# Kernel optimization log

Hardware: AMD Instinct MI355X
Metric: run time of the kernel (lower is better)

## Reference

```python
import jax, jax.numpy as jnp
import numpy as np

# sizes
N, B, NPG = 8192, 8, 1024          # total nodes, graphs, nodes per graph (equal-size graphs)
D, H, DH, L = 256, 8, 32, 2        # hidden, heads, head dim, layers
IN_C, OUT_D, E, DFF = 128, 64, 262144, 512
EPS = 1e-5


def setup_inputs() -> dict:
    key = jax.random.key(0)
    ks = jax.random.split(key, 20)
    p = lambda i, shp: jax.random.normal(ks[i], shp, jnp.float32) * 0.05
    return dict(
        x=jax.random.normal(ks[0], (N, IN_C), jnp.float32),
        edge_index=jax.random.randint(ks[1], (2, E), 0, N),
        batch=jnp.arange(N, dtype=jnp.int32) // NPG,  # sorted, equal-size graphs
        w_in=p(2, (D, IN_C)), b_in=p(3, (D,)),
        sage_wl=p(4, (L, D, D)), sage_bl=p(5, (L, D)), sage_wr=p(6, (L, D, D)),
        attn_iw=p(7, (L, 3 * D, D)), attn_ib=p(8, (L, 3 * D)),
        attn_ow=p(9, (L, D, D)), attn_ob=p(10, (L, D)),
        n1_w=jnp.ones((L, D)), n1_b=jnp.zeros((L, D)),
        n2_w=jnp.ones((L, D)), n2_b=jnp.zeros((L, D)),
        n3_w=jnp.ones((L, D)), n3_b=jnp.zeros((L, D)),
        mlp_w1=p(11, (L, DFF, D)), mlp_b1=p(12, (L, DFF)),
        mlp_w2=p(13, (L, D, DFF)), mlp_b2=p(14, (L, D)),
        bn_w=jnp.ones((L, D)), bn_b=jnp.zeros((L, D)),
        w_out=p(15, (OUT_D, D)), b_out=p(16, (OUT_D,)),
    )


def _bn(h, w, b):
    # BatchNorm1d over nodes (training-mode batch statistics, biased var)
    m = h.mean(0)
    v = jnp.mean((h - m) ** 2, axis=0)
    return (h - m) * jax.lax.rsqrt(v + EPS) * w + b


def _forward(x, edge_index, batch, w_in, b_in, sage_wl, sage_bl, sage_wr,
             attn_iw, attn_ib, attn_ow, attn_ob, n1_w, n1_b, n2_w, n2_b,
             n3_w, n3_b, mlp_w1, mlp_b1, mlp_w2, mlp_b2, bn_w, bn_b, w_out, b_out):
    src, dst = edge_index[0], edge_index[1]
    deg = jax.ops.segment_sum(jnp.ones((E,), jnp.float32), dst, num_segments=N)
    inv_deg = (1.0 / jnp.clip(deg, 1.0))[:, None]
    scale = 1.0 / np.sqrt(DH)

    h = x @ w_in.T + b_in  # in_proj Linear  [N, D]
    for l in range(L):
        # --- GPSConv: local SAGEConv (mean aggr) + residual + norm1 ---
        agg = jax.ops.segment_sum(h[src], dst, num_segments=N) * inv_deg
        loc = agg @ sage_wl[l].T + sage_bl[l] + h @ sage_wr[l].T
        loc = _bn(loc + h, n1_w[l], n1_b[l])
        # --- GPSConv: dense per-graph multi-head self-attention + residual + norm2 ---
        hd = h.reshape(B, NPG, D)  # to_dense_batch (no padding: equal graph sizes)
        qkv = hd @ attn_iw[l].T + attn_ib[l]  # [B, n, 3D]
        q, k, v = jnp.split(qkv, 3, axis=-1)
        sh = lambda t: t.reshape(B, NPG, H, DH).transpose(0, 2, 1, 3)  # [B, H, n, DH]
        a = jax.nn.softmax(jnp.einsum('bhqd,bhkd->bhqk', sh(q) * scale, sh(k)), axis=-1)
        o = jnp.einsum('bhqk,bhkd->bhqd', a, sh(v)).transpose(0, 2, 1, 3).reshape(B, NPG, D)
        o = (o @ attn_ow[l].T + attn_ob[l]).reshape(N, D)
        glob = _bn(o + h, n2_w[l], n2_b[l])
        # --- GPSConv: sum branches, MLP residual, norm3 ---
        out = loc + glob
        out = out + jax.nn.relu(out @ mlp_w1[l].T + mlp_b1[l]) @ mlp_w2[l].T + mlp_b2[l]
        out = _bn(out, n3_w[l], n3_b[l])
        # --- outer GPS: BatchNorm + relu + (dropout=eval) + residual ---
        h = h + jax.nn.relu(_bn(out, bn_w[l], bn_b[l]))
    pooled = h.reshape(B, NPG, D).mean(axis=1)  # global_mean_pool over sorted equal-size graphs
    return pooled @ w_out.T + b_out  # [B, OUT_D]


def reference(x, edge_index, batch, w_in, b_in, sage_wl, sage_bl, sage_wr,
              attn_iw, attn_ib, attn_ow, attn_ob, n1_w, n1_b, n2_w, n2_b,
              n3_w, n3_b, mlp_w1, mlp_b1, mlp_w2, mlp_b2, bn_w, bn_b, w_out, b_out):
    return _forward(x, edge_index, batch, w_in, b_in, sage_wl, sage_bl, sage_wr,
                    attn_iw, attn_ib, attn_ow, attn_ob, n1_w, n1_b, n2_w, n2_b,
                    n3_w, n3_b, mlp_w1, mlp_b1, mlp_w2, mlp_b2, bn_w, bn_b, w_out, b_out)
```

## Files before the change

kernel.cpp:

```cpp
#include <hip/hip_runtime.h>
#include <hip/hip_bf16.h>

#define N_NODES 8192
#define BGRAPH 8
#define NPG 1024
#define DIM 256
#define NH 8
#define DHEAD 32
#define NLAYERS 2
#define INC 128
#define OUTD 64
#define NEDGE 262144
#define DFF 512
#define EPS 1e-5f

typedef __attribute__((ext_vector_type(4))) float f32x4;
typedef __attribute__((ext_vector_type(8))) short s16x8;
typedef __attribute__((ext_vector_type(4))) ushort u16x4;

__device__ __forceinline__ float b2f(ushort u){
  unsigned v = ((unsigned)u) << 16;
  return __builtin_bit_cast(float, v);
}
__device__ __forceinline__ ushort f2b(float f){
  unsigned u = __builtin_bit_cast(unsigned, f);
  u += 0x7fffu + ((u >> 16) & 1u);
  return (ushort)(u >> 16);
}
__device__ __forceinline__ ushort f2b_trunc(float f){
  return (ushort)(__builtin_bit_cast(unsigned, f) >> 16);
}
__device__ __forceinline__ void gload16(const void* g, void* l){
  __builtin_amdgcn_global_load_lds(
    (const __attribute__((address_space(1))) void*)g,
    (__attribute__((address_space(3))) void*)l,
    16, 0, 0);
}

#define CX  1048576
#define CWI (CX+32768)
#define CSW (CWI+262144)
#define CIW (CSW+393216)
#define COW (CIW+131072)
#define CW1 (COW+262144)
#define CW2 (CW1+262144)
#define NCAST (CW2/256)
__global__ void k_setup(const float* __restrict__ x, const float* __restrict__ w_in,
    const float* __restrict__ wl, const float* __restrict__ wr,
    const float* __restrict__ iw, const float* __restrict__ ow,
    const float* __restrict__ w1, const float* __restrict__ w2,
    ushort* __restrict__ dst, const int* __restrict__ edst, int* __restrict__ deg){
  if(blockIdx.x >= NCAST){
    int i = (blockIdx.x - NCAST)*256 + threadIdx.x;
    int stride = 512*256;
    for(; i<NEDGE; i+=stride) atomicAdd(&deg[edst[i]], 1);
    return;
  }
  int i = blockIdx.x*256 + threadIdx.x;
  float val;
  if(i < CX)       val = x[i];
  else if(i < CWI) val = w_in[i-CX];
  else if(i < CSW){
    int j = i - CWI;
    int l = j >> 17, r = (j >> 9) & 255, k = j & 511;
    val = (k < 256) ? wl[(l<<16) + (r<<8) + k] : wr[(l<<16) + (r<<8) + (k-256)];
  }
  else if(i < CIW) val = iw[i-CSW];
  else if(i < COW) val = ow[i-CIW];
  else if(i < CW1) val = w1[i-COW];
  else             val = w2[i-CW1];
  dst[i] = f2b(val);
}

__global__ void k_scan(const int* __restrict__ deg, int* __restrict__ offs,
                       float* __restrict__ inv_deg){
  __shared__ int s[1024];
  int t = threadIdx.x;
  int base = t*8;
  int loc[8]; int acc=0;
  #pragma unroll
  for(int j=0;j<8;j++){
    int dv = deg[base+j];
    inv_deg[base+j] = 1.0f/(float)(dv>0?dv:1);
    loc[j]=acc; acc += dv;
  }
  s[t]=acc;
  __syncthreads();
  for(int d=1; d<1024; d<<=1){
    int v = (t>=d)? s[t-d] : 0;
    __syncthreads();
    if(t>=d) s[t]+=v;
    __syncthreads();
  }
  int pre = (t>0)? s[t-1] : 0;
  #pragma unroll
  for(int j=0;j<8;j++) offs[base+j] = pre + loc[j];
  if(t==1023) offs[N_NODES] = s[1023];
}

#define STAGE_AB(t, buf) do{ \
    int kt_ = (t)*64; \
    _Pragma("unroll") \
    for(int it=0; it<2; ++it){ \
      int c = (wave*2+it)*64 + lane; \
      int row = c >> 3, q = c & 7; \
      int qs = q ^ (row & 7); \
      gload16(A + (size_t)(bm+row)*lda + kt_ + qs*8, (char*)As + (buf)*8192 + (wave*2+it)*1024); \
      gload16(W + (size_t)(bn+row)*K   + kt_ + qs*8, (char*)Bs + (buf)*8192 + (wave*2+it)*1024); \
    } \
  }while(0)

#define MM_COMPUTE(BUFOFF) \
      _Pragma("unroll") \
      for(int kk=0; kk<2; ++kk){ \
        s16x8 af[2], bfr[2]; \
        _Pragma("unroll") \
        for(int mi=0; mi<2; ++mi){ \
          int row = wr*32 + mi*16 + l15; \
          int col = (kk*64 + l4*16) ^ ((row & 7) << 4); \
          af[mi] = *(const s16x8*)((const char*)As + (BUFOFF) + row*128 + col); \
        } \
        _Pragma("unroll") \
        for(int nj=0; nj<2; ++nj){ \
          int row = wc*32 + nj*16 + l15; \
          int col = (kk*64 + l4*16) ^ ((row & 7) << 4); \
          bfr[nj] = *(const s16x8*)((const char*)Bs + (BUFOFF) + row*128 + col); \
        } \
        _Pragma("unroll") \
        for(int mi=0; mi<2; ++mi) \
          _Pragma("unroll") \
          for(int nj=0; nj<2; ++nj) \
            acc[mi][nj] = __builtin_amdgcn_mfma_f32_16x16x32_bf16(af[mi], bfr[nj], acc[mi][nj], 0,0,0); \
      }

#define MM_LOOP \
  f32x4 acc[2][2] = {}; \
  { const int nt = K >> 6; \
    STAGE_AB(0, 0); \
    asm volatile("s_waitcnt vmcnt(0)" ::: "memory"); \
    __builtin_amdgcn_s_barrier(); \
    int cur = 0; \
    for(int t=0; t<nt; ++t){ \
      if(t+1 < nt) STAGE_AB(t+1, cur^1); \
      MM_COMPUTE(cur*8192) \
      asm volatile("s_waitcnt vmcnt(0)" ::: "memory"); \
      __builtin_amdgcn_s_barrier(); \
      cur ^= 1; \
    } \
  }

#define MM_LOOP_SB \
  f32x4 acc[2][2] = {}; \
  { const int nt = K >> 6; \
    for(int t=0; t<nt; ++t){ \
      __syncthreads(); \
      STAGE_AB(t, 0); \
      asm volatile("s_waitcnt vmcnt(0)" ::: "memory"); \
      __builtin_amdgcn_s_barrier(); \
      MM_COMPUTE(0) \
    } \
  }

template<bool RELU, bool RESID, bool RESIDB, bool BIAS, bool WF32, bool WBF, bool STATS>
__global__ __launch_bounds__(256) void k_mm(const ushort* __restrict__ A,
    const ushort* __restrict__ W, const float* __restrict__ bias,
    const float* __restrict__ resid, const ushort* __restrict__ residb,
    float* __restrict__ Cf, ushort* __restrict__ Cb,
    float* __restrict__ gS, float* __restrict__ gQ,
    int M, int Nc, int K, int lda, int ldcb)
{
  __shared__ ushort As[2*64*64];
  __shared__ ushort Bs[2*64*64];
  __shared__ float sredS[64];
  __shared__ float sredQ[64];
  const int tid = threadIdx.x;
  const int lane = tid & 63, wave = tid >> 6;
  const int l15 = lane & 15, l4 = lane >> 4;
  const int bm = blockIdx.y*64, bn = blockIdx.x*64;
  const int wr = wave >> 1, wc = wave & 1;
  MM_LOOP

  float sloc[2] = {0.f,0.f}, qloc[2] = {0.f,0.f};
  #pragma unroll
  for(int mi=0; mi<2; ++mi){
    #pragma unroll
    for(int nj=0; nj<2; ++nj){
      int col = bn + wc*32 + nj*16 + l15;
      float bv = BIAS ? bias[col] : 0.f;
      #pragma unroll
      for(int r=0; r<4; ++r){
        int row = bm + wr*32 + mi*16 + l4*4 + r;
        size_t off = (size_t)row*Nc + col;
        float v = acc[mi][nj][r] + bv;
        if(RESID)  v += resid[off];
        if(RESIDB) v += b2f(residb[off]);
        if(RELU)   v = fmaxf(v, 0.f);
        if(WF32)   Cf[off] = v;
        if(WBF)    Cb[(size_t)row*ldcb + col] = f2b(v);
        if(STATS){ sloc[nj] += v; qloc[nj] += v*v; }
      }
    }
  }
  if(STATS){
    if(tid < 64){ sredS[tid]=0.f; sredQ[tid]=0.f; }
    __syncthreads();
    int c0 = wc*32 + l15;
    atomicAdd(&sredS[c0],    sloc[0]); atomicAdd(&sredQ[c0],    qloc[0]);
    atomicAdd(&sredS[c0+16], sloc[1]); atomicAdd(&sredQ[c0+16], qloc[1]);
    __syncthreads();
    if(tid < 64){
      atomicAdd(&gS[bn+tid], sredS[tid]);
      atomicAdd(&gQ[bn+tid], sredQ[tid]);
    }
  }
}

__global__ __launch_bounds__(256) void k_fill_inproj(const int* __restrict__ src,
    const int* __restrict__ dst, const int* __restrict__ offs,
    int* __restrict__ cursor, int* __restrict__ csr,
    const ushort* __restrict__ xb, const ushort* __restrict__ w_in_b,
    const float* __restrict__ b_in, float* __restrict__ H,
    ushort* __restrict__ hwb)
{
  __shared__ __align__(16) char smem[16384];
  const int tid = threadIdx.x;
  if(blockIdx.x < 512){
    int i = blockIdx.x*256 + tid;
    for(; i<NEDGE; i+=512*256){
      int d = dst[i];
      int p = atomicAdd(&cursor[d], 1);
      csr[offs[d]+p] = src[i];
    }
  } else {
    int idx = blockIdx.x - 512;
    const int lane = tid & 63, wave = tid >> 6;
    const int l15 = lane & 15, l4 = lane >> 4;
    const int bn = (idx & 3)*64, bm = (idx >> 2)*64;
    const int wr = wave >> 1, wc = wave & 1;
    const ushort* A = xb;
    const ushort* W = w_in_b;
    const int K = INC, lda = INC;
    ushort* As = (ushort*)smem;
    ushort* Bs = As + 4096;
    MM_LOOP_SB
    #pragma unroll
    for(int mi=0; mi<2; ++mi){
      #pragma unroll
      for(int nj=0; nj<2; ++nj){
        int col = bn + wc*32 + nj*16 + l15;
        float bv = b_in[col];
        #pragma unroll
        for(int r=0; r<4; ++r){
          int row = bm + wr*32 + mi*16 + l4*4 + r;
          float v = acc[mi][nj][r] + bv;
          H[(size_t)row*DIM + col] = v;
          hwb[(size_t)row*512 + 256 + col] = f2b(v);
        }
      }
    }
  }
}

__global__ __launch_bounds__(256) void k_agg_qkv(ushort* __restrict__ hwb,
    const int* __restrict__ offs, const int* __restrict__ csr,
    const float* __restrict__ inv_deg, const ushort* __restrict__ iwb,
    const float* __restrict__ attn_ib, ushort* __restrict__ qpack,
    ushort* __restrict__ kpack, ushort* __restrict__ vpack)
{
  __shared__ __align__(16) char smem[16384];
  const int tid = threadIdx.x;
  const int lane = tid & 63, wave = tid >> 6;
  if(blockIdx.x < 2048){
    int n = blockIdx.x*4 + wave;
    int beg = offs[n], end = offs[n+1];
    f32x4 a0 = {0,0,0,0}, a1 = {0,0,0,0}, a2 = {0,0,0,0}, a3 = {0,0,0,0};
    int i = beg;
    for(; i+4<=end; i+=4){
      int j0=csr[i], j1=csr[i+1], j2=csr[i+2], j3=csr[i+3];
      u16x4 v0 = *(const u16x4*)(hwb + (size_t)j0*512 + 256 + lane*4);
      u16x4 v1 = *(const u16x4*)(hwb + (size_t)j1*512 + 256 + lane*4);
      u16x4 v2 = *(const u16x4*)(hwb + (size_t)j2*512 + 256 + lane*4);
      u16x4 v3 = *(const u16x4*)(hwb + (size_t)j3*512 + 256 + lane*4);
      #pragma unroll
      for(int c=0;c<4;c++){ a0[c]+=b2f(v0[c]); a1[c]+=b2f(v1[c]);
                            a2[c]+=b2f(v2[c]); a3[c]+=b2f(v3[c]); }
    }
    for(; i<end; ++i){
      int j0=csr[i];
      u16x4 v0 = *(const u16x4*)(hwb + (size_t)j0*512 + 256 + lane*4);
      #pragma unroll
      for(int c=0;c<4;c++) a0[c]+=b2f(v0[c]);
    }
    float inv = inv_deg[n];
    u16x4 outv;
    #pragma unroll
    for(int c=0;c<4;c++) outv[c] = f2b((a0[c]+a1[c]+a2[c]+a3[c])*inv);
    *(u16x4*)(hwb + (size_t)n*512 + lane*4) = outv;
  } else {
    int idx = blockIdx.x - 2048;
    const int bn = (idx % 12)*64, bm = (idx / 12)*64;
    const int l15 = lane & 15, l4 = lane >> 4;
    const int wr = wave >> 1, wc = wave & 1;
    const ushort* A = hwb + 256;
    const ushort* W = iwb;
    const int K = 256, lda = 512;
    ushort* As = (ushort*)smem;
    ushort* Bs = As + 4096;
    MM_LOOP_SB
    const int bgq = bm >> 10;
    #pragma unroll
    for(int mi=0; mi<2; ++mi){
      #pragma unroll
      for(int nj=0; nj<2; ++nj){
        int col = bn + wc*32 + nj*16 + l15;
        float bv = attn_ib[col];
        int part = col >> 8;
        int hh = (col >> 5) & 7;
        int dd = col & 31;
        ushort* dstp = (part==0 ? qpack : (part==1 ? kpack : vpack))
                     + (size_t)(bgq*8 + hh)*32768 + dd;
        #pragma unroll
        for(int r=0; r<4; ++r){
          int rig = (bm + wr*32 + mi*16 + l4*4 + r) & 1023;
          dstp[rig*32] = f2b(acc[mi][nj][r] + bv);
        }
      }
    }
  }
}

__global__ __launch_bounds__(256) void k_attn_sage(const ushort* __restrict__ qpack,
    const ushort* __restrict__ kpack, const ushort* __restrict__ vpack,
    ushort* __restrict__ attnO, const ushort* __restrict__ hwb,
    const ushort* __restrict__ swb, const float* __restrict__ sage_bl,
    const float* __restrict__ H, ushort* __restrict__ locB,
    float* __restrict__ gS, float* __restrict__ gQ)
{
  __shared__ __align__(16) char smem[20992];
  const int tid = threadIdx.x;
  const int lane = tid & 63, wave = tid >> 6;
  const int l15 = lane & 15;
  if(blockIdx.x < 1024){
    ushort* KsB = (ushort*)smem;
    ushort* VtB = (ushort*)smem + 6144;
    const int g = lane >> 4;
    int bid = blockIdx.x;
    int h  = bid & 7;
    int bg = (bid >> 3) & 7;
    int qc = bid >> 6;
    const int bgh = bid & 63;
    const int nb = bg*NPG + qc*64 + wave*16;
    const ushort* qp = qpack + (size_t)bgh*32768;
    const ushort* kp = kpack + (size_t)bgh*32768;
    const ushort* vp = vpack + (size_t)bgh*32768;

    const int rho = tid >> 2, qq = tid & 3;
    const int grp = rho >> 5, r32 = rho & 31;
    const int tt = r32 >> 4, wi = r32 & 15;
    const int jperm = grp*32 + (wi >> 2)*8 + tt*4 + (wi & 3);
    const int qs = qq ^ ((rho >> 1) & 3);

    s16x8 qf = *(const s16x8*)(qp + (qc*64 + wave*16 + l15)*32 + g*8);
    {
      const float scale2 = 0.2550370703637335f;
      #pragma unroll
      for(int i=0;i<8;i++) qf[i] = (short)f2b(b2f((ushort)qf[i]) * scale2);
    }
    f32x4 o0 = {0.f,0.f,0.f,0.f}, o1 = {0.f,0.f,0.f,0.f};
    float mrun = -1e30f, lrun = 0.f;

    gload16(kp + (size_t)jperm*32 + qs*8, (char*)KsB + wave*1024);
    s16x8 vcur = *(const s16x8*)(vp + (size_t)lane*32 + wave*8);

    for(int st=0; st<16; ++st){
      int vb = st & 1;
      int kbuf = st % 3;
      ushort* vtb = VtB + vb*2048;
      #pragma unroll
      for(int i=0;i<8;i++){
        int d = wave*8 + i;
        vtb[d*64 + (lane ^ (i<<3))] = (ushort)vcur[i];
      }
      s16x8 vnext = vcur;
      if(st+1 < 16){
        gload16(kp + (size_t)((st+1)*64 + jperm)*32 + qs*8,
                (char*)(KsB + ((st+1)%3)*2048) + wave*1024);
        vnext = *(const s16x8*)(vp + (size_t)((st+1)*64 + lane)*32 + wave*8);
      }
      asm volatile("s_waitcnt lgkmcnt(0)" ::: "memory");
      __builtin_amdgcn_s_barrier();

      const char* ksb = (const char*)(KsB + kbuf*2048);
      f32x4 sc[4];
      __builtin_amdgcn_s_setprio(1);
      #pragma unroll
      for(int q4=0; q4<4; ++q4){
        int r0 = q4*16 + l15;
        s16x8 kf = *(const s16x8*)(ksb + r0*64 + ((g*16) ^ (((r0>>1)&3)<<4)));
        f32x4 z = {0.f,0.f,0.f,0.f};
        sc[q4] = __builtin_amdgcn_mfma_f32_16x16x32_bf16(kf, qf, z, 0,0,0);
      }
      __builtin_amdgcn_s_setprio(0);

      float smax = -1e30f;
      #pragma unroll
      for(int q4=0; q4<4; ++q4)
        #pragma unroll
        for(int r=0; r<4; ++r) smax = fmaxf(smax, sc[q4][r]);
      smax = fmaxf(smax, __shfl_xor(smax, 16));
      smax = fmaxf(smax, __shfl_xor(smax, 32));

      if(!__all((int)(smax <= mrun + 8.0f))){
        float mnew = fmaxf(mrun, smax);
        float alpha = exp2f(mrun - mnew);
        lrun *= alpha;
        #pragma unroll
        for(int r=0;r<4;r++){
          float ar = __shfl(alpha, (lane & 48) | (g*4 + r), 64);
          o0[r] *= ar; o1[r] *= ar;
        }
        mrun = mnew;
      }

      float p[16];
      float ps = 0.f;
      #pragma unroll
      for(int q4=0; q4<4; ++q4)
        #pragma unroll
        for(int r=0; r<4; ++r){
          float pv = exp2f(sc[q4][r] - mrun);
          p[q4*4+r] = pv; ps += pv;
        }
      ps += __shfl_xor(ps, 16);
      ps += __shfl_xor(ps, 32);
      lrun += ps;

      s16x8 pa0, pa1;
      #pragma unroll
      for(int i=0;i<8;i++){ pa0[i] = (short)f2b_trunc(p[i]); pa1[i] = (short)f2b_trunc(p[8+i]); }

      const char* vtc = (const char*)(VtB + vb*2048);
      int colb0 = g*16, colb1 = 64 + g*16;
      int d0 = l15, d1 = l15 + 16;
      s16x8 v00 = *(const s16x8*)(vtc + d0*128 + (colb0 ^ ((d0&7)<<4)));
      s16x8 v01 = *(const s16x8*)(vtc + d1*128 + (colb0 ^ ((d1&7)<<4)));
      s16x8 v10 = *(const s16x8*)(vtc + d0*128 + (colb1 ^ ((d0&7)<<4)));
      s16x8 v11 = *(const s16x8*)(vtc + d1*128 + (colb1 ^ ((d1&7)<<4)));
      __builtin_amdgcn_s_setprio(1);
      o0 = __builtin_amdgcn_mfma_f32_16x16x32_bf16(pa0, v00, o0, 0,0,0);
      o1 = __builtin_amdgcn_mfma_f32_16x16x32_bf16(pa0, v01, o1, 0,0,0);
      o0 = __builtin_amdgcn_mfma_f32_16x16x32_bf16(pa1, v10, o0, 0,0,0);
      o1 = __builtin_amdgcn_mfma_f32_16x16x32_bf16(pa1, v11, o1, 0,0,0);
      __builtin_amdgcn_s_setprio(0);

      vcur = vnext;
    }
    float inv = 1.0f/lrun;
    #pragma unroll
    for(int r=0;r<4;r++){
      int q2 = g*4 + r;
      float ir = __shfl(inv, (lane & 48) | q2, 64);
      size_t nrow = (size_t)(nb + q2)*DIM + h*32;
      attnO[nrow + l15]      = f2b(o0[r]*ir);
      attnO[nrow + 16 + l15] = f2b(o1[r]*ir);
    }
  } else {
    int idx = blockIdx.x - 1024;
    const int bn = (idx & 3)*64, bm = (idx >> 2)*64;
    const int l4 = lane >> 4;
    const int wr = wave >> 1, wc = wave & 1;
    const ushort* A = hwb;
    const ushort* W = swb;
    const int K = 512, lda = 512;
    ushort* As = (ushort*)smem;
    ushort* Bs = As + 4096;
    float* sredS = (float*)(smem + 16384);
    float* sredQ = sredS + 64;
    MM_LOOP_SB

    float sloc[2] = {0.f,0.f}, qloc[2] = {0.f,0.f};
    #pragma unroll
    for(int mi=0; mi<2; ++mi){
      #pragma unroll
      for(int nj=0; nj<2; ++nj){
        int col = bn + wc*32 + nj*16 + l15;
        float bv = sage_bl[col];
        #pragma unroll
        for(int r=0; r<4; ++r){
          int row = bm + wr*32 + mi*16 + l4*4 + r;
          size_t off = (size_t)row*DIM + col;
          float v = acc[mi][nj][r] + bv + H[off];
          locB[off] = f2b(v);
          sloc[nj] += v; qloc[nj] += v*v;
        }
      }
    }
    if(tid < 64){ sredS[tid]=0.f; sredQ[tid]=0.f; }
    __syncthreads();
    int c0 = wc*32 + l15;
    atomicAdd(&sredS[c0],    sloc[0]); atomicAdd(&sredQ[c0],    qloc[0]);
    atomicAdd(&sredS[c0+16], sloc[1]); atomicAdd(&sredQ[c0+16], qloc[1]);
    __syncthreads();
    if(tid < 64){
      atomicAdd(&gS[bn+tid], sredS[tid]);
      atomicAdd(&gQ[bn+tid], sredQ[tid]);
    }
  }
}

__global__ __launch_bounds__(256) void k_apply12(const ushort* __restrict__ locB,
    const ushort* __restrict__ globB, const float* __restrict__ slot,
    const float* __restrict__ n1w, const float* __restrict__ n1b,
    const float* __restrict__ n2w, const float* __restrict__ n2b,
    ushort* __restrict__ combB){
  int t = blockIdx.x*256 + threadIdx.x;
  int base = t*4;
  int d0 = base & 255;
  u16x4 lv = *(const u16x4*)(locB + base);
  u16x4 gv = *(const u16x4*)(globB + base);
  f32x4 s1 = *(const f32x4*)(slot + d0);
  f32x4 q1 = *(const f32x4*)(slot + 256 + d0);
  f32x4 s2 = *(const f32x4*)(slot + 512 + d0);
  f32x4 q2 = *(const f32x4*)(slot + 768 + d0);
  f32x4 w1v = *(const f32x4*)(n1w + d0);
  f32x4 b1v = *(const f32x4*)(n1b + d0);
  f32x4 w2v = *(const f32x4*)(n2w + d0);
  f32x4 b2v = *(const f32x4*)(n2b + d0);
  const float invn = 1.0f/N_NODES;
  u16x4 outv;
  #pragma unroll
  for(int c=0;c<4;c++){
    float m1 = s1[c]*invn, v1 = q1[c]*invn - m1*m1;
    float m2 = s2[c]*invn, v2 = q2[c]*invn - m2*m2;
    float y1 = (b2f(lv[c])-m1)*rsqrtf(v1+EPS)*w1v[c] + b1v[c];
    float y2 = (b2f(gv[c])-m2)*rsqrtf(v2+EPS)*w2v[c] + b2v[c];
    outv[c] = f2b(y1 + y2);
  }
  *(u16x4*)(combB + base) = outv;
}

__global__ __launch_bounds__(256) void k_apply3o(const ushort* __restrict__ xB,
    const float* __restrict__ slot, const float* __restrict__ n3w,
    const float* __restrict__ bw, const float* __restrict__ bb,
    float* __restrict__ H, ushort* __restrict__ hwbR){
  int t = blockIdx.x*256 + threadIdx.x;
  int base = t*4;
  int d0 = base & 255;
  int row = base >> 8;
  u16x4 xv = *(const u16x4*)(xB + base);
  f32x4 s3 = *(const f32x4*)(slot + 1024 + d0);
  f32x4 q3 = *(const f32x4*)(slot + 1280 + d0);
  f32x4 wv3 = *(const f32x4*)(n3w + d0);
  f32x4 bwv = *(const f32x4*)(bw + d0);
  f32x4 bbv = *(const f32x4*)(bb + d0);
  f32x4 hv = *(f32x4*)(H + base);
  const float invn = 1.0f/N_NODES;
  u16x4 outv;
  #pragma unroll
  for(int c=0;c<4;c++){
    float m = s3[c]*invn, var = q3[c]*invn - m*m;
    float rs = rsqrtf(var+EPS);
    float gch = rs*wv3[c];
    float rso = rsqrtf(gch*gch*var + EPS);
    float yo = (b2f(xv[c])-m)*gch*rso*bwv[c] + bbv[c];
    float h = hv[c] + fmaxf(yo, 0.f);
    hv[c] = h;
    outv[c] = f2b(h);
  }
  *(f32x4*)(H + base) = hv;
  *(u16x4*)(hwbR + (size_t)row*512 + d0) = outv;
}

__global__ void k_pool(const float* __restrict__ h, float* __restrict__ pooled){
  int b = blockIdx.x, c = blockIdx.y, d = threadIdx.x;
  int r0 = c*64;
  float s=0.f;
  for(int i=0;i<64;i++) s += h[(size_t)(b*NPG + r0 + i)*DIM + d];
  atomicAdd(&pooled[b*DIM+d], s*(1.0f/NPG));
}
__global__ void k_out(const float* __restrict__ pooled, const float* __restrict__ w_out,
                      const float* __restrict__ b_out, float* __restrict__ out){
  int t = threadIdx.x;
  if(t >= BGRAPH*OUTD) return;
  int b = t/OUTD, oc = t%OUTD;
  float s = b_out[oc];
  for(int k=0;k<DIM;k++) s += pooled[b*DIM+k]*w_out[oc*DIM+k];
  out[t] = s;
}

extern "C" void kernel_launch(void* const* d_in, const int* in_sizes, int n_in,
                              void* d_out, int out_size, void* d_ws, size_t ws_size,
                              hipStream_t stream) {
  const float* x       = (const float*)d_in[0];
  const int*   edge    = (const int*)d_in[1];
  const float* w_in    = (const float*)d_in[3];
  const float* b_in    = (const float*)d_in[4];
  const float* sage_wl = (const float*)d_in[5];
  const float* sage_bl = (const float*)d_in[6];
  const float* sage_wr = (const float*)d_in[7];
  const float* attn_iw = (const float*)d_in[8];
  const float* attn_ib = (const float*)d_in[9];
  const float* attn_ow = (const float*)d_in[10];
  const float* attn_ob = (const float*)d_in[11];
  const float* n1_w = (const float*)d_in[12];
  const float* n1_b = (const float*)d_in[13];
  const float* n2_w = (const float*)d_in[14];
  const float* n2_b = (const float*)d_in[15];
  const float* n3_w = (const float*)d_in[16];
  const float* n3_b = (const float*)d_in[17];
  const float* mlp_w1 = (const float*)d_in[18];
  const float* mlp_b1 = (const float*)d_in[19];
  const float* mlp_w2 = (const float*)d_in[20];
  const float* mlp_b2 = (const float*)d_in[21];
  const float* bn_w = (const float*)d_in[22];
  const float* bn_b = (const float*)d_in[23];
  const float* w_out = (const float*)d_in[24];
  const float* b_out = (const float*)d_in[25];

  const size_t ND = (size_t)N_NODES*DIM;
  float* ws    = (float*)d_ws;
  float* H     = ws;
  ushort* wsb   = (ushort*)(ws + ND);
  ushort* locB  = wsb;
  ushort* globB = wsb + ND;
  ushort* hwb   = wsb + 2*ND;
  ushort* qpack = wsb + 4*ND;
  ushort* kpack = wsb + 5*ND;
  ushort* vpack = wsb + 6*ND;
  ushort* attnOb= wsb + 7*ND;
  ushort* combb = wsb + 8*ND;
  ushort* hidb  = wsb + 9*ND;
  ushort* castb = wsb + 11*ND;
  ushort* xb     = castb;
  ushort* w_in_b = castb + CX;
  ushort* sageWb = castb + CWI;
  ushort* iw_b   = castb + CSW;
  ushort* ow_b   = castb + CIW;
  ushort* w1_b   = castb + COW;
  ushort* w2_b   = castb + CW1;
  float* mf      = (float*)(castb + CW2);
  float* inv_deg = mf;
  float* bnslots = mf + 8192;
  float* pooled  = bnslots + 3072;
  int* deg    = (int*)(pooled + 2048);
  int* cursor = deg + N_NODES;
  int* offs   = cursor + N_NODES;
  int* csr    = offs + N_NODES + 8;

  const int* esrc = edge;
  const int* edst = edge + NEDGE;

  hipMemsetAsync(bnslots, 0, (3072+2048)*sizeof(float) + 2*N_NODES*sizeof(int), stream);

  k_setup<<<NCAST+512,256,0,stream>>>(x, w_in, sage_wl, sage_wr, attn_iw,
      attn_ow, mlp_w1, mlp_w2, castb, edst, deg);
  k_scan<<<1,1024,0,stream>>>(deg, offs, inv_deg);

  k_fill_inproj<<<1024,256,0,stream>>>(esrc, edst, offs, cursor, csr,
      xb, w_in_b, b_in, H, hwb);

  for(int l=0; l<NLAYERS; ++l){
    const ushort* swb = sageWb + (size_t)l*131072;
    const ushort* iwb = iw_b + (size_t)l*196608;
    const ushort* owb = ow_b + (size_t)l*65536;
    const ushort* w1b = w1_b + (size_t)l*131072;
    const ushort* w2b = w2_b + (size_t)l*131072;
    float* slot = bnslots + (size_t)l*1536;

    k_agg_qkv<<<3584,256,0,stream>>>(hwb, offs, csr, inv_deg, iwb,
        attn_ib + l*3*DIM, qpack, kpack, vpack);

    k_attn_sage<<<1536,256,0,stream>>>(qpack, kpack, vpack, attnOb, hwb, swb,
        sage_bl + l*DIM, H, locB, slot, slot+256);

    k_mm<false,true,false,true,false,true,true><<<dim3(4,128),256,0,stream>>>(
        attnOb, owb, attn_ob + l*DIM, H, nullptr, nullptr, globB, slot+512, slot+768,
        N_NODES, DIM, DIM, DIM, DIM);

    k_apply12<<<2048,256,0,stream>>>(locB, globB, slot,
        n1_w + l*DIM, n1_b + l*DIM, n2_w + l*DIM, n2_b + l*DIM, combb);

    k_mm<true,false,false,true,false,true,false><<<dim3(8,128),256,0,stream>>>(
        combb, w1b, mlp_b1 + l*DFF, nullptr, nullptr, nullptr, hidb,
        nullptr, nullptr, N_NODES, DFF, DIM, DIM, 512);
    k_mm<false,false,true,true,false,true,true><<<dim3(4,128),256,0,stream>>>(
        hidb, w2b, mlp_b2 + l*DIM, nullptr, combb, nullptr, globB,
        slot+1024, slot+1280, N_NODES, DIM, 512, 512, DIM);

    k_apply3o<<<2048,256,0,stream>>>(globB, slot, n3_w + l*DIM,
        bn_w + l*DIM, bn_b + l*DIM, H, hwb+256);
  }

  k_pool<<<dim3(BGRAPH, NPG/64),256,0,stream>>>(H, pooled);
  k_out<<<1,512,0,stream>>>(pooled, w_out, b_out, (float*)d_out);
}
```

Baseline: 262.3 us.

## Drop fp32 residual stream and fuse BN1/BN2 apply into MLP1 GEMM

The fp32 hidden-state buffer H is removed, and the bf16 copy in hwb now serves as the residual everywhere: sage epilogue, out-proj residual, apply3o, and pooling. The separate BN1+BN2 elementwise kernel is folded into the first MLP GEMM, which normalises locB/globB on the fly while staging A tiles. The x==0 column blocks also write combB for the later residual. This saves fp32 traffic and one launch, but the A operand is now recomputed by all eight column blocks and the residual accumulates in bf16, which lowers precision across layers.

```diff
diff --git a/kernel.cpp b/kernel.cpp
--- a/kernel.cpp
+++ b/kernel.cpp
@@ -161,13 +161,12 @@
     } \
   }
 
-template<bool RELU, bool RESID, bool RESIDB, bool BIAS, bool WF32, bool WBF, bool STATS>
+template<bool RELU, bool RESIDB, bool BIAS, bool WBF, bool STATS>
 __global__ __launch_bounds__(256) void k_mm(const ushort* __restrict__ A,
     const ushort* __restrict__ W, const float* __restrict__ bias,
-    const float* __restrict__ resid, const ushort* __restrict__ residb,
-    float* __restrict__ Cf, ushort* __restrict__ Cb,
+    const ushort* __restrict__ residb, ushort* __restrict__ Cb,
     float* __restrict__ gS, float* __restrict__ gQ,
-    int M, int Nc, int K, int lda, int ldcb)
+    int M, int Nc, int K, int lda, int ldcb, int ldrb)
 {
   __shared__ ushort As[2*64*64];
   __shared__ ushort Bs[2*64*64];
@@ -190,12 +189,9 @@
       #pragma unroll
       for(int r=0; r<4; ++r){
         int row = bm + wr*32 + mi*16 + l4*4 + r;
-        size_t off = (size_t)row*Nc + col;
         float v = acc[mi][nj][r] + bv;
-        if(RESID)  v += resid[off];
-        if(RESIDB) v += b2f(residb[off]);
+        if(RESIDB) v += b2f(residb[(size_t)row*ldrb + col]);
         if(RELU)   v = fmaxf(v, 0.f);
-        if(WF32)   Cf[off] = v;
         if(WBF)    Cb[(size_t)row*ldcb + col] = f2b(v);
         if(STATS){ sloc[nj] += v; qloc[nj] += v*v; }
       }
@@ -219,8 +215,7 @@
     const int* __restrict__ dst, const int* __restrict__ offs,
     int* __restrict__ cursor, int* __restrict__ csr,
     const ushort* __restrict__ xb, const ushort* __restrict__ w_in_b,
-    const float* __restrict__ b_in, float* __restrict__ H,
-    ushort* __restrict__ hwb)
+    const float* __restrict__ b_in, ushort* __restrict__ hwb)
 {
   __shared__ __align__(16) char smem[16384];
   const int tid = threadIdx.x;
@@ -252,9 +247,7 @@
         #pragma unroll
         for(int r=0; r<4; ++r){
           int row = bm + wr*32 + mi*16 + l4*4 + r;
-          float v = acc[mi][nj][r] + bv;
-          H[(size_t)row*DIM + col] = v;
-          hwb[(size_t)row*512 + 256 + col] = f2b(v);
+          hwb[(size_t)row*512 + 256 + col] = f2b(acc[mi][nj][r] + bv);
         }
       }
     }
@@ -333,8 +326,7 @@
     const ushort* __restrict__ kpack, const ushort* __restrict__ vpack,
     ushort* __restrict__ attnO, const ushort* __restrict__ hwb,
     const ushort* __restrict__ swb, const float* __restrict__ sage_bl,
-    const float* __restrict__ H, ushort* __restrict__ locB,
-    float* __restrict__ gS, float* __restrict__ gQ)
+    ushort* __restrict__ locB, float* __restrict__ gS, float* __restrict__ gQ)
 {
   __shared__ __align__(16) char smem[20992];
   const int tid = threadIdx.x;
@@ -488,9 +480,8 @@
         #pragma unroll
         for(int r=0; r<4; ++r){
           int row = bm + wr*32 + mi*16 + l4*4 + r;
-          size_t off = (size_t)row*DIM + col;
-          float v = acc[mi][nj][r] + bv + H[off];
-          locB[off] = f2b(v);
+          float v = acc[mi][nj][r] + bv + b2f(hwb[(size_t)row*512 + 256 + col]);
+          locB[(size_t)row*DIM + col] = f2b(v);
           sloc[nj] += v; qloc[nj] += v*v;
         }
       }
@@ -508,52 +499,98 @@
   }
 }
 
-__global__ __launch_bounds__(256) void k_apply12(const ushort* __restrict__ locB,
+__global__ __launch_bounds__(256) void k_bn12_mlp1(const ushort* __restrict__ locB,
     const ushort* __restrict__ globB, const float* __restrict__ slot,
     const float* __restrict__ n1w, const float* __restrict__ n1b,
     const float* __restrict__ n2w, const float* __restrict__ n2b,
-    ushort* __restrict__ combB){
-  int t = blockIdx.x*256 + threadIdx.x;
-  int base = t*4;
-  int d0 = base & 255;
-  u16x4 lv = *(const u16x4*)(locB + base);
-  u16x4 gv = *(const u16x4*)(globB + base);
-  f32x4 s1 = *(const f32x4*)(slot + d0);
-  f32x4 q1 = *(const f32x4*)(slot + 256 + d0);
-  f32x4 s2 = *(const f32x4*)(slot + 512 + d0);
-  f32x4 q2 = *(const f32x4*)(slot + 768 + d0);
-  f32x4 w1v = *(const f32x4*)(n1w + d0);
-  f32x4 b1v = *(const f32x4*)(n1b + d0);
-  f32x4 w2v = *(const f32x4*)(n2w + d0);
-  f32x4 b2v = *(const f32x4*)(n2b + d0);
-  const float invn = 1.0f/N_NODES;
-  u16x4 outv;
+    const ushort* __restrict__ w1b, const float* __restrict__ mlp_b1,
+    ushort* __restrict__ combB, ushort* __restrict__ hidb)
+{
+  __shared__ __align__(16) ushort As[4096];
+  __shared__ __align__(16) ushort Bs[4096];
+  __shared__ float pA1[256], pA2[256], pCC[256];
+  const int tid = threadIdx.x;
+  const int lane = tid & 63, wave = tid >> 6;
+  const int l15 = lane & 15, l4 = lane >> 4;
+  const int bm = blockIdx.y*64, bn = blockIdx.x*64;
+  const int wr = wave >> 1, wc = wave & 1;
+  const int K = 256;
+  {
+    int d = tid;
+    const float invn = 1.0f/N_NODES;
+    float m1 = slot[d]*invn,     v1 = slot[256+d]*invn - m1*m1;
+    float m2 = slot[512+d]*invn, v2 = slot[768+d]*invn - m2*m2;
+    float a1 = rsqrtf(v1+EPS)*n1w[d];
+    float a2 = rsqrtf(v2+EPS)*n2w[d];
+    pA1[d] = a1; pA2[d] = a2;
+    pCC[d] = (n1b[d] - m1*a1) + (n2b[d] - m2*a2);
+  }
+  f32x4 acc[2][2] = {};
+  for(int t=0; t<4; ++t){
+    int kt = t*64;
+    __syncthreads();
+    #pragma unroll
+    for(int it=0; it<2; ++it){
+      int c = (wave*2+it)*64 + lane;
+      int row = c >> 3, q = c & 7;
+      int qs = q ^ (row & 7);
+      gload16(w1b + (size_t)(bn+row)*K + kt + qs*8, (char*)Bs + (wave*2+it)*1024);
+    }
+    #pragma unroll
+    for(int it=0; it<2; ++it){
+      int c = (wave*2+it)*64 + lane;
+      int row = c >> 3, q = c & 7;
+      int qs = q ^ (row & 7);
+      int gr = bm + row;
+      int k0 = kt + qs*8;
+      u16x4 lv0 = *(const u16x4*)(locB  + (size_t)gr*256 + k0);
+      u16x4 lv1 = *(const u16x4*)(locB  + (size_t)gr*256 + k0 + 4);
+      u16x4 gv0 = *(const u16x4*)(globB + (size_t)gr*256 + k0);
+      u16x4 gv1 = *(const u16x4*)(globB + (size_t)gr*256 + k0 + 4);
+      s16x8 pk;
+      #pragma unroll
+      for(int e=0;e<4;e++){
+        pk[e]   = (short)f2b(pA1[k0+e]  *b2f(lv0[e]) + pA2[k0+e]  *b2f(gv0[e]) + pCC[k0+e]);
+        pk[4+e] = (short)f2b(pA1[k0+4+e]*b2f(lv1[e]) + pA2[k0+4+e]*b2f(gv1[e]) + pCC[k0+4+e]);
+      }
+      *(s16x8*)((char*)As + c*16) = pk;
+      if(blockIdx.x == 0)
+        *(s16x8*)(combB + (size_t)gr*256 + k0) = pk;
+    }
+    asm volatile("s_waitcnt vmcnt(0) lgkmcnt(0)" ::: "memory");
+    __builtin_amdgcn_s_barrier();
+    MM_COMPUTE(0)
+  }
   #pragma unroll
-  for(int c=0;c<4;c++){
-    float m1 = s1[c]*invn, v1 = q1[c]*invn - m1*m1;
-    float m2 = s2[c]*invn, v2 = q2[c]*invn - m2*m2;
-    float y1 = (b2f(lv[c])-m1)*rsqrtf(v1+EPS)*w1v[c] + b1v[c];
-    float y2 = (b2f(gv[c])-m2)*rsqrtf(v2+EPS)*w2v[c] + b2v[c];
-    outv[c] = f2b(y1 + y2);
-  }
-  *(u16x4*)(combB + base) = outv;
+  for(int mi=0; mi<2; ++mi){
+    #pragma unroll
+    for(int nj=0; nj<2; ++nj){
+      int col = bn + wc*32 + nj*16 + l15;
+      float bv = mlp_b1[col];
+      #pragma unroll
+      for(int r=0; r<4; ++r){
+        int row = bm + wr*32 + mi*16 + l4*4 + r;
+        hidb[(size_t)row*512 + col] = f2b(fmaxf(acc[mi][nj][r] + bv, 0.f));
+      }
+    }
+  }
 }
 
 __global__ __launch_bounds__(256) void k_apply3o(const ushort* __restrict__ xB,
     const float* __restrict__ slot, const float* __restrict__ n3w,
     const float* __restrict__ bw, const float* __restrict__ bb,
-    float* __restrict__ H, ushort* __restrict__ hwbR){
+    ushort* __restrict__ hwbR){
   int t = blockIdx.x*256 + threadIdx.x;
   int base = t*4;
   int d0 = base & 255;
   int row = base >> 8;
   u16x4 xv = *(const u16x4*)(xB + base);
+  u16x4 hv = *(const u16x4*)(hwbR + (size_t)row*512 + d0);
   f32x4 s3 = *(const f32x4*)(slot + 1024 + d0);
   f32x4 q3 = *(const f32x4*)(slot + 1280 + d0);
   f32x4 wv3 = *(const f32x4*)(n3w + d0);
   f32x4 bwv = *(const f32x4*)(bw + d0);
   f32x4 bbv = *(const f32x4*)(bb + d0);
-  f32x4 hv = *(f32x4*)(H + base);
   const float invn = 1.0f/N_NODES;
   u16x4 outv;
   #pragma unroll
@@ -563,19 +600,16 @@
     float gch = rs*wv3[c];
     float rso = rsqrtf(gch*gch*var + EPS);
     float yo = (b2f(xv[c])-m)*gch*rso*bwv[c] + bbv[c];
-    float h = hv[c] + fmaxf(yo, 0.f);
-    hv[c] = h;
-    outv[c] = f2b(h);
-  }
-  *(f32x4*)(H + base) = hv;
+    outv[c] = f2b(b2f(hv[c]) + fmaxf(yo, 0.f));
+  }
   *(u16x4*)(hwbR + (size_t)row*512 + d0) = outv;
 }
 
-__global__ void k_pool(const float* __restrict__ h, float* __restrict__ pooled){
+__global__ void k_pool(const ushort* __restrict__ hwbR, float* __restrict__ pooled){
   int b = blockIdx.x, c = blockIdx.y, d = threadIdx.x;
   int r0 = c*64;
   float s=0.f;
-  for(int i=0;i<64;i++) s += h[(size_t)(b*NPG + r0 + i)*DIM + d];
+  for(int i=0;i<64;i++) s += b2f(hwbR[(size_t)(b*NPG + r0 + i)*512 + d]);
   atomicAdd(&pooled[b*DIM+d], s*(1.0f/NPG));
 }
 __global__ void k_out(const float* __restrict__ pooled, const float* __restrict__ w_out,
@@ -618,9 +652,7 @@
   const float* b_out = (const float*)d_in[25];
 
   const size_t ND = (size_t)N_NODES*DIM;
-  float* ws    = (float*)d_ws;
-  float* H     = ws;
-  ushort* wsb   = (ushort*)(ws + ND);
+  ushort* wsb   = (ushort*)d_ws;
   ushort* locB  = wsb;
   ushort* globB = wsb + ND;
   ushort* hwb   = wsb + 2*ND;
@@ -657,7 +689,7 @@
   k_scan<<<1,1024,0,stream>>>(deg, offs, inv_deg);
 
   k_fill_inproj<<<1024,256,0,stream>>>(esrc, edst, offs, cursor, csr,
-      xb, w_in_b, b_in, H, hwb);
+      xb, w_in_b, b_in, hwb);
 
   for(int l=0; l<NLAYERS; ++l){
     const ushort* swb = sageWb + (size_t)l*131072;
@@ -671,26 +703,24 @@
         attn_ib + l*3*DIM, qpack, kpack, vpack);
 
     k_attn_sage<<<1536,256,0,stream>>>(qpack, kpack, vpack, attnOb, hwb, swb,
-        sage_bl + l*DIM, H, locB, slot, slot+256);
-
-    k_mm<false,true,false,true,false,true,true><<<dim3(4,128),256,0,stream>>>(
-        attnOb, owb, attn_ob + l*DIM, H, nullptr, nullptr, globB, slot+512, slot+768,
-        N_NODES, DIM, DIM, DIM, DIM);
-
-    k_apply12<<<2048,256,0,stream>>>(locB, globB, slot,
-        n1_w + l*DIM, n1_b + l*DIM, n2_w + l*DIM, n2_b + l*DIM, combb);
-
-    k_mm<true,false,false,true,false,true,false><<<dim3(8,128),256,0,stream>>>(
-        combb, w1b, mlp_b1 + l*DFF, nullptr, nullptr, nullptr, hidb,
-        nullptr, nullptr, N_NODES, DFF, DIM, DIM, 512);
-    k_mm<false,false,true,true,false,true,true><<<dim3(4,128),256,0,stream>>>(
-        hidb, w2b, mlp_b2 + l*DIM, nullptr, combb, nullptr, globB,
-        slot+1024, slot+1280, N_NODES, DIM, 512, 512, DIM);
+        sage_bl + l*DIM, locB, slot, slot+256);
+
+    k_mm<false,true,true,true,true><<<dim3(4,128),256,0,stream>>>(
+        attnOb, owb, attn_ob + l*DIM, hwb+256, globB, slot+512, slot+768,
+        N_NODES, DIM, DIM, DIM, DIM, 512);
+
+    k_bn12_mlp1<<<dim3(8,128),256,0,stream>>>(locB, globB, slot,
+        n1_w + l*DIM, n1_b + l*DIM, n2_w + l*DIM, n2_b + l*DIM,
+        w1b, mlp_b1 + l*DFF, combb, hidb);
+
+    k_mm<false,true,true,true,true><<<dim3(4,128),256,0,stream>>>(
+        hidb, w2b, mlp_b2 + l*DIM, combb, globB, slot+1024, slot+1280,
+        N_NODES, DIM, 512, 512, DIM, 256);
 
     k_apply3o<<<2048,256,0,stream>>>(globB, slot, n3_w + l*DIM,
-        bn_w + l*DIM, bn_b + l*DIM, H, hwb+256);
-  }
-
-  k_pool<<<dim3(BGRAPH, NPG/64),256,0,stream>>>(H, pooled);
+        bn_w + l*DIM, bn_b + l*DIM, hwb+256);
+  }
+
+  k_pool<<<dim3(BGRAPH, NPG/64),256,0,stream>>>(hwb+256, pooled);
   k_out<<<1,512,0,stream>>>(pooled, w_out, b_out, (float*)d_out);
 }
```

Result: no change. 267.0 us (+1.8%).
